# Optimization experiments

Measured on AMD Instinct MI355X. Metric: run time of the kernel, lower is better.

The kernel has to match this reference:

```python
import jax, jax.numpy as jnp
import numpy as np

B, C, H, W = 4, 64, 64, 64
CQ = C // 8

def setup_inputs() -> dict:
    key = jax.random.key(0)
    ks = jax.random.split(key, 8)
    s = 1.0 / np.sqrt(C)
    return {
        "x": jax.random.normal(ks[0], (B, C, H, W), dtype=jnp.float32),
        "Wq": jax.random.normal(ks[1], (CQ, C), dtype=jnp.float32) * s,
        "bq": jax.random.normal(ks[2], (CQ,), dtype=jnp.float32) * 0.01,
        "Wk": jax.random.normal(ks[3], (CQ, C), dtype=jnp.float32) * s,
        "bk": jax.random.normal(ks[4], (CQ,), dtype=jnp.float32) * 0.01,
        "Wv": jax.random.normal(ks[5], (C, C), dtype=jnp.float32) * s,
        "bv": jax.random.normal(ks[6], (C,), dtype=jnp.float32) * 0.01,
        "gamma": jax.random.normal(ks[7], (1,), dtype=jnp.float32) * 0.1,
    }

def reference(x, Wq, bq, Wk, bk, Wv, bv, gamma):
    b, c, h, w = x.shape
    n = h * w
    xf = x.reshape(b, c, n)  # [B, C, N]
    # 1x1 convs are pointwise channel projections
    q = jnp.einsum('oc,bcn->bon', Wq, xf) + bq[None, :, None]  # [B, CQ, N]
    k = jnp.einsum('oc,bcn->bon', Wk, xf) + bk[None, :, None]  # [B, CQ, N]
    v = jnp.einsum('oc,bcn->bon', Wv, xf) + bv[None, :, None]  # [B, C, N]
    energy = jnp.einsum('bcn,bcm->bnm', q, k)                  # [B, N, N]
    attn = jax.nn.softmax(energy, axis=-1)
    out = jnp.einsum('bcm,bnm->bcn', v, attn)                  # [B, C, N]
    out = out.reshape(b, c, h, w)
    return gamma[0] * out + x
```

## Files before the change

kernel.cpp:

```cpp
#include <hip/hip_runtime.h>
#include <hip/hip_bf16.h>


typedef __attribute__((ext_vector_type(8))) short short8;
typedef __attribute__((ext_vector_type(4))) float f32x4;
typedef __attribute__((ext_vector_type(4))) unsigned uint4v;
typedef unsigned short ushort_t;

#define NSEQ 4096
#define LOG2E 1.4426950408889634f

__device__ __forceinline__ unsigned pk_bf16(float lo, float hi) {
  const unsigned short a = __builtin_bit_cast(unsigned short, __float2bfloat16(lo));
  const unsigned short b = __builtin_bit_cast(unsigned short, __float2bfloat16(hi));
  return (unsigned)a | ((unsigned)b << 16);
}

__global__ __launch_bounds__(256, 4) void proj_kernel(
    const float* __restrict__ x,
    const float* __restrict__ Wq, const float* __restrict__ bq,
    const float* __restrict__ Wk, const float* __restrict__ bk,
    const float* __restrict__ Wv, const float* __restrict__ bv,
    ushort_t* __restrict__ Qb, ushort_t* __restrict__ Kb,
    ushort_t* __restrict__ Vb)
{
  const int tid  = threadIdx.x;
  const int lane = tid & 63;
  const int w    = __builtin_amdgcn_readfirstlane(tid >> 6);
  const int blk  = blockIdx.x;
  const int quarter = blk & 3;
  const int g    = (blk >> 2) & 63;
  const int b    = blk >> 8;
  const int n    = g * 64 + lane;

  const float* xb = x + (size_t)(b * 64) * NSEQ + n;
  const int co0 = quarter * 16 + w * 4;
  const float* w0 = Wv + (co0 + 0) * 64;
  const float* w1 = Wv + (co0 + 1) * 64;
  const float* w2 = Wv + (co0 + 2) * 64;
  const float* w3 = Wv + (co0 + 3) * 64;
  const int p = quarter * 4 + w;
  const float* wr = (p < 8) ? (Wq + p * 64) : (Wk + (p - 8) * 64);
  float a0 = bv[co0 + 0], a1 = bv[co0 + 1], a2 = bv[co0 + 2], a3 = bv[co0 + 3];
  float aq = (p < 8) ? bq[p] : bk[p - 8];

#pragma unroll
  for (int kc = 0; kc < 64; kc += 8) {
    float xv[8];
#pragma unroll
    for (int i = 0; i < 8; ++i) xv[i] = xb[(size_t)(kc + i) * NSEQ];
#pragma unroll
    for (int i = 0; i < 8; ++i) {
      const float xk = xv[i];
      a0 += w0[kc + i] * xk;
      a1 += w1[kc + i] * xk;
      a2 += w2[kc + i] * xk;
      a3 += w3[kc + i] * xk;
      aq += wr[kc + i] * xk;
    }
  }

  ushort_t* vt = Vb + ((size_t)(b * 128 + (n >> 5)) * 64 + co0) * 32 + (n & 31);
  vt[0]  = __builtin_bit_cast(ushort_t, __float2bfloat16(a0));
  vt[32] = __builtin_bit_cast(ushort_t, __float2bfloat16(a1));
  vt[64] = __builtin_bit_cast(ushort_t, __float2bfloat16(a2));
  vt[96] = __builtin_bit_cast(ushort_t, __float2bfloat16(a3));

  if (p < 8) aq *= LOG2E;
  ushort_t* qk = ((p < 8) ? Qb : Kb) + ((size_t)(b * NSEQ + n)) * 8 + (p & 7);
  *qk = __builtin_bit_cast(ushort_t, __float2bfloat16(aq));
}

__global__ __launch_bounds__(512, 2) void attn_kernel(
    const ushort_t* __restrict__ Qb, const ushort_t* __restrict__ Kb,
    const ushort_t* __restrict__ Vb, const float* __restrict__ x,
    const float* __restrict__ gamma, float* __restrict__ out)
{
  __shared__ float buf[4][64][69];

  const int tid  = threadIdx.x;
  const int wave = __builtin_amdgcn_readfirstlane(tid >> 6);
  const int lane = tid & 63;
  const int q16  = lane & 15;
  const int quad = lane >> 4;
  const int blk  = blockIdx.x;
  const int b    = blk >> 6;
  const int n0   = (blk & 63) << 6;
  const int mbase = wave << 9;

  const short8 z8 = {0, 0, 0, 0, 0, 0, 0, 0};
  short8 qf[4];
#pragma unroll
  for (int qt = 0; qt < 4; ++qt) {
    qf[qt] = *(const short8*)(Qb + ((size_t)(b * NSEQ + n0 + qt * 16 + q16)) * 8);
    if (quad != 0) qf[qt] = z8;
  }

  const int mperm = 8 * (q16 >> 2) + (q16 & 3);
  const char* kbase = (const char*)(Kb + ((size_t)(b * NSEQ + mbase + mperm)) * 8);
  const char* vbase = (const char*)(Vb + ((size_t)(b * 128 + (mbase >> 5)) * 64) * 32)
                      + q16 * 64 + quad * 16;

  f32x4 acc[4][4];
#pragma unroll
  for (int qt = 0; qt < 4; ++qt)
#pragma unroll
    for (int cf = 0; cf < 4; ++cf) acc[qt][cf] = (f32x4){0.f, 0.f, 0.f, 0.f};
  float l[4] = {0.f, 0.f, 0.f, 0.f};

#pragma unroll 1
  for (int t = 0; t < 16; ++t) {
    const char* kp = kbase + (size_t)t * 512;
    const char* vp = vbase + (size_t)t * 4096;
    const short8 kf0 = *(const short8*)(kp);
    const short8 kf1 = *(const short8*)(kp + 64);
    const short8 vf0 = *(const short8*)(vp);
    const short8 vf1 = *(const short8*)(vp + 1024);
    const short8 vf2 = *(const short8*)(vp + 2048);
    const short8 vf3 = *(const short8*)(vp + 3072);

#pragma unroll
    for (int qt = 0; qt < 4; ++qt) {
      const f32x4 z = {0.f, 0.f, 0.f, 0.f};
      f32x4 s0 = __builtin_amdgcn_mfma_f32_16x16x32_bf16(kf0, qf[qt], z, 0, 0, 0);
      f32x4 s1 = __builtin_amdgcn_mfma_f32_16x16x32_bf16(kf1, qf[qt], z, 0, 0, 0);

      const float p0 = __builtin_amdgcn_exp2f(s0[0]);
      const float p1 = __builtin_amdgcn_exp2f(s0[1]);
      const float p2 = __builtin_amdgcn_exp2f(s0[2]);
      const float p3 = __builtin_amdgcn_exp2f(s0[3]);
      const float p4 = __builtin_amdgcn_exp2f(s1[0]);
      const float p5 = __builtin_amdgcn_exp2f(s1[1]);
      const float p6 = __builtin_amdgcn_exp2f(s1[2]);
      const float p7 = __builtin_amdgcn_exp2f(s1[3]);
      l[qt] += ((p0 + p1) + (p2 + p3)) + ((p4 + p5) + (p6 + p7));

      const uint4v u = {pk_bf16(p0, p1), pk_bf16(p2, p3),
                        pk_bf16(p4, p5), pk_bf16(p6, p7)};
      const short8 pf = __builtin_bit_cast(short8, u);

      acc[qt][0] = __builtin_amdgcn_mfma_f32_16x16x32_bf16(vf0, pf, acc[qt][0], 0, 0, 0);
      acc[qt][1] = __builtin_amdgcn_mfma_f32_16x16x32_bf16(vf1, pf, acc[qt][1], 0, 0, 0);
      acc[qt][2] = __builtin_amdgcn_mfma_f32_16x16x32_bf16(vf2, pf, acc[qt][2], 0, 0, 0);
      acc[qt][3] = __builtin_amdgcn_mfma_f32_16x16x32_bf16(vf3, pf, acc[qt][3], 0, 0, 0);
    }
  }

#pragma unroll
  for (int qt = 0; qt < 4; ++qt) {
    l[qt] += __shfl_xor(l[qt], 16);
    l[qt] += __shfl_xor(l[qt], 32);
  }

  if (wave >= 4) {
    float* d = &buf[wave - 4][lane][0];
#pragma unroll
    for (int qt = 0; qt < 4; ++qt) {
#pragma unroll
      for (int cf = 0; cf < 4; ++cf)
#pragma unroll
        for (int r = 0; r < 4; ++r) d[qt * 16 + cf * 4 + r] = acc[qt][cf][r];
      d[64 + qt] = l[qt];
    }
  }
  __syncthreads();
  if (wave < 4) {
    float* d = &buf[wave][lane][0];
#pragma unroll
    for (int qt = 0; qt < 4; ++qt) {
#pragma unroll
      for (int cf = 0; cf < 4; ++cf)
#pragma unroll
        for (int r = 0; r < 4; ++r) {
          acc[qt][cf][r] += d[qt * 16 + cf * 4 + r];
          d[qt * 16 + cf * 4 + r] = acc[qt][cf][r];
        }
      l[qt] += d[64 + qt];
      d[64 + qt] = l[qt];
    }
  }
  __syncthreads();

  const int qt = wave >> 1;
  const int cg0 = (wave & 1) * 2;
  float lt = 0.f;
#pragma unroll
  for (int w2 = 0; w2 < 4; ++w2) lt += buf[w2][lane][64 + qt];
  const float ginv = gamma[0] / lt;
  const int nn = n0 + qt * 16 + q16;

#pragma unroll
  for (int h = 0; h < 2; ++h) {
    const int cg = cg0 + h;
    float fr[4] = {0.f, 0.f, 0.f, 0.f};
#pragma unroll
    for (int w2 = 0; w2 < 4; ++w2)
#pragma unroll
      for (int r = 0; r < 4; ++r) fr[r] += buf[w2][lane][qt * 16 + cg * 4 + r];
#pragma unroll
    for (int r = 0; r < 4; ++r) {
      const int c = cg * 16 + quad * 4 + r;
      const size_t idx = ((size_t)(b * 64 + c)) * NSEQ + nn;
      out[idx] = fr[r] * ginv + x[idx];
    }
  }
}

extern "C" void kernel_launch(void* const* d_in, const int* in_sizes, int n_in,
                              void* d_out, int out_size, void* d_ws, size_t ws_size,
                              hipStream_t stream) {
  (void)in_sizes; (void)n_in; (void)out_size; (void)ws_size;
  const float* x     = (const float*)d_in[0];
  const float* Wq    = (const float*)d_in[1];
  const float* bq    = (const float*)d_in[2];
  const float* Wk    = (const float*)d_in[3];
  const float* bk    = (const float*)d_in[4];
  const float* Wv    = (const float*)d_in[5];
  const float* bv    = (const float*)d_in[6];
  const float* gamma = (const float*)d_in[7];
  float* out = (float*)d_out;

  ushort_t* Qb = (ushort_t*)d_ws;
  ushort_t* Kb = (ushort_t*)((char*)d_ws + (256u << 10));
  ushort_t* Vb = (ushort_t*)((char*)d_ws + (512u << 10));

  hipLaunchKernelGGL(proj_kernel, dim3(1024), dim3(256), 0, stream,
                     x, Wq, bq, Wk, bk, Wv, bv, Qb, Kb, Vb);
  hipLaunchKernelGGL(attn_kernel, dim3(256), dim3(512), 0, stream,
                     Qb, Kb, Vb, x, gamma, out);
}
```

Baseline: 95.22 us.

## Prefetch next K/V tile and compute softmax row sums via MFMA with ones

Software-pipelines the attention loop by loading the next iteration's K and V fragments before computing the current one, with the loop unrolled by two, so global-load latency overlaps with MFMA and exp work. It also replaces the scalar VALU sum of exponentials and the cross-lane shuffles with an extra MFMA that multiplies the bf16 probabilities by a ones matrix. This moves the reduction onto the matrix unit and frees VALU cycles. In exchange it adds register pressure from the prefetched fragments and the extra accumulator, and the row sums are now taken from bf16-rounded probabilities.

```diff
diff --git a/kernel.cpp b/kernel.cpp
--- a/kernel.cpp
+++ b/kernel.cpp
@@ -96,28 +96,42 @@
     if (quad != 0) qf[qt] = z8;
   }
 
+  const short one_bf = (short)0x3F80;
+  const short8 ones = {one_bf, one_bf, one_bf, one_bf,
+                       one_bf, one_bf, one_bf, one_bf};
+
   const int mperm = 8 * (q16 >> 2) + (q16 & 3);
   const char* kbase = (const char*)(Kb + ((size_t)(b * NSEQ + mbase + mperm)) * 8);
   const char* vbase = (const char*)(Vb + ((size_t)(b * 128 + (mbase >> 5)) * 64) * 32)
                       + q16 * 64 + quad * 16;
 
   f32x4 acc[4][4];
-#pragma unroll
-  for (int qt = 0; qt < 4; ++qt)
+  f32x4 lacc[4];
+#pragma unroll
+  for (int qt = 0; qt < 4; ++qt) {
+    lacc[qt] = (f32x4){0.f, 0.f, 0.f, 0.f};
 #pragma unroll
     for (int cf = 0; cf < 4; ++cf) acc[qt][cf] = (f32x4){0.f, 0.f, 0.f, 0.f};
-  float l[4] = {0.f, 0.f, 0.f, 0.f};
-
-#pragma unroll 1
+  }
+
+  short8 kf0 = *(const short8*)(kbase);
+  short8 kf1 = *(const short8*)(kbase + 64);
+  short8 vf0 = *(const short8*)(vbase);
+  short8 vf1 = *(const short8*)(vbase + 1024);
+  short8 vf2 = *(const short8*)(vbase + 2048);
+  short8 vf3 = *(const short8*)(vbase + 3072);
+
+#pragma unroll 2
   for (int t = 0; t < 16; ++t) {
-    const char* kp = kbase + (size_t)t * 512;
-    const char* vp = vbase + (size_t)t * 4096;
-    const short8 kf0 = *(const short8*)(kp);
-    const short8 kf1 = *(const short8*)(kp + 64);
-    const short8 vf0 = *(const short8*)(vp);
-    const short8 vf1 = *(const short8*)(vp + 1024);
-    const short8 vf2 = *(const short8*)(vp + 2048);
-    const short8 vf3 = *(const short8*)(vp + 3072);
+    const int tn = (t + 1 < 16) ? (t + 1) : 15;
+    const char* kp = kbase + (size_t)tn * 512;
+    const char* vp = vbase + (size_t)tn * 4096;
+    const short8 nk0 = *(const short8*)(kp);
+    const short8 nk1 = *(const short8*)(kp + 64);
+    const short8 nv0 = *(const short8*)(vp);
+    const short8 nv1 = *(const short8*)(vp + 1024);
+    const short8 nv2 = *(const short8*)(vp + 2048);
+    const short8 nv3 = *(const short8*)(vp + 3072);
 
 #pragma unroll
     for (int qt = 0; qt < 4; ++qt) {
@@ -133,7 +147,6 @@
       const float p5 = __builtin_amdgcn_exp2f(s1[1]);
       const float p6 = __builtin_amdgcn_exp2f(s1[2]);
       const float p7 = __builtin_amdgcn_exp2f(s1[3]);
-      l[qt] += ((p0 + p1) + (p2 + p3)) + ((p4 + p5) + (p6 + p7));
 
       const uint4v u = {pk_bf16(p0, p1), pk_bf16(p2, p3),
                         pk_bf16(p4, p5), pk_bf16(p6, p7)};
@@ -143,14 +156,16 @@
       acc[qt][1] = __builtin_amdgcn_mfma_f32_16x16x32_bf16(vf1, pf, acc[qt][1], 0, 0, 0);
       acc[qt][2] = __builtin_amdgcn_mfma_f32_16x16x32_bf16(vf2, pf, acc[qt][2], 0, 0, 0);
       acc[qt][3] = __builtin_amdgcn_mfma_f32_16x16x32_bf16(vf3, pf, acc[qt][3], 0, 0, 0);
-    }
-  }
-
-#pragma unroll
-  for (int qt = 0; qt < 4; ++qt) {
-    l[qt] += __shfl_xor(l[qt], 16);
-    l[qt] += __shfl_xor(l[qt], 32);
-  }
+      lacc[qt]   = __builtin_amdgcn_mfma_f32_16x16x32_bf16(ones, pf, lacc[qt], 0, 0, 0);
+    }
+
+    kf0 = nk0; kf1 = nk1;
+    vf0 = nv0; vf1 = nv1; vf2 = nv2; vf3 = nv3;
+  }
+
+  float l[4];
+#pragma unroll
+  for (int qt = 0; qt < 4; ++qt) l[qt] = lacc[qt][0];
 
   if (wave >= 4) {
     float* d = &buf[wave - 4][lane][0];
```

Measured after the change: 98.23 us. 3.2% more time.
